# Kernel optimization log

Measured on AMD Instinct MI355X. Metric: run time of the kernel, lower is better.

Reference implementation:

```python
import jax, jax.numpy as jnp
import numpy as np

RADIUS = 0.1
MAX_EDGES = 4_194_304  # cap on total neighbor pairs (expected ~1.1M)

def _cdist(a, b):
    # pairwise Euclidean distances: [M,3] x [N,3] -> [M,N]
    a2 = jnp.sum(a * a, axis=-1, keepdims=True)          # [M,1]
    b2 = jnp.sum(b * b, axis=-1, keepdims=True).T        # [1,N]
    d2 = a2 + b2 - 2.0 * (a @ b.T)
    return jnp.sqrt(jnp.maximum(d2, 0.0))


def setup_inputs() -> dict:
    key = jax.random.key(0)
    k1, k2 = jax.random.split(key)
    inp_positions = jax.random.uniform(k1, (16384, 3), dtype=jnp.float32)
    out_positions = jax.random.uniform(k2, (16384, 3), dtype=jnp.float32)
    return {"inp_positions": inp_positions, "out_positions": out_positions}


def reference(inp_positions, out_positions):
    M = out_positions.shape[0]
    N = inp_positions.shape[0]
    distances = _cdist(out_positions, inp_positions)      # [M,N]
    mask = distances <= RADIUS                            # [M,N] bool
    # jit-compatible nonzero: flatten, fixed-size output, sentinel fill M*N
    flat_idx = jnp.nonzero(mask.ravel(), size=MAX_EDGES, fill_value=M * N)[0]
    query_index = flat_idx // N                           # padded slots -> M (out of range sentinel)
    neighbors_index = jnp.where(flat_idx < M * N, flat_idx % N, -1)
    # bincount(query_index, minlength=M) == row-wise sum of mask
    counts = jnp.sum(mask, axis=1)                        # [M] int32
    row_splits = jnp.pad(jnp.cumsum(counts), (1, 0))      # [M+1]
    return neighbors_index, row_splits
```

## Files before the change

kernel.cpp:

```cpp
#include <hip/hip_runtime.h>
#include <math.h>

typedef float f32x2 __attribute__((ext_vector_type(2)));

constexpr int M_ROWS    = 16384;
constexpr int N_PTS     = 16384;
constexpr int MAX_EDGES = 4194304;

constexpr int TPB    = 256;
constexpr int RPT    = 8;
constexpr int NPAIR  = RPT / 2;
constexpr int NCHUNK = 256;
constexpr int CHUNK  = N_PTS / NCHUNK;
constexpr int WPC    = CHUNK / 32;
constexpr int ROWS_PER_BLOCK = TPB * RPT;
constexpr int RB     = M_ROWS / ROWS_PER_BLOCK;
constexpr int CGRP   = 16;
constexpr int NGRP   = NCHUNK / CGRP;

static __device__ __forceinline__ f32x2 pk_fma(f32x2 a, f32x2 b, f32x2 c) {
#if __has_builtin(__builtin_elementwise_fma)
    return __builtin_elementwise_fma(a, b, c);
#else
    f32x2 r; r.x = __fmaf_rn(a.x, b.x, c.x); r.y = __fmaf_rn(a.y, b.y, c.y); return r;
#endif
}

static __device__ __forceinline__ void bitstep(unsigned& m, float t, float tr) {
    asm("v_cmp_le_f32 vcc, %1, %2\n\t"
        "v_addc_co_u32 %0, vcc, %0, %0, vcc"
        : "+v"(m) : "v"(t), "v"(tr) : "vcc");
}

__global__ void __launch_bounds__(TPB)
mask_count_kernel(const float* __restrict__ inp, const float* __restrict__ outp,
                  unsigned* __restrict__ mask, unsigned char* __restrict__ cchunk,
                  float T) {
    int rb = blockIdx.x / NCHUNK;
    int c  = blockIdx.x % NCHUNK;
    int t  = threadIdx.x;
    __shared__ f32x2 sb[CHUNK * 4];
    if (t < CHUNK) {
        int j = c * CHUNK + t;
        float x = inp[j * 3 + 0], y = inp[j * 3 + 1], z = inp[j * 3 + 2];
        float s = __fadd_rn(__fadd_rn(__fmul_rn(x, x), __fmul_rn(y, y)), __fmul_rn(z, z));
        float nx = -2.0f * x, ny = -2.0f * y, nz = -2.0f * z;
        sb[t * 4 + 0] = (f32x2){nx, nx};
        sb[t * 4 + 1] = (f32x2){ny, ny};
        sb[t * 4 + 2] = (f32x2){nz, nz};
        sb[t * 4 + 3] = (f32x2){s, s};
    }
    __syncthreads();
    int row0 = rb * ROWS_PER_BLOCK + t;
    f32x2 ax[NPAIR], ay[NPAIR], az[NPAIR], Tr[NPAIR];
#pragma unroll
    for (int k = 0; k < NPAIR; ++k) {
        int r0 = row0 + (2 * k) * TPB;
        int r1 = row0 + (2 * k + 1) * TPB;
        float x0 = outp[r0 * 3 + 0], y0 = outp[r0 * 3 + 1], z0 = outp[r0 * 3 + 2];
        float x1 = outp[r1 * 3 + 0], y1 = outp[r1 * 3 + 1], z1 = outp[r1 * 3 + 2];
        float w0 = __fadd_rn(__fadd_rn(__fmul_rn(x0, x0), __fmul_rn(y0, y0)), __fmul_rn(z0, z0));
        float w1 = __fadd_rn(__fadd_rn(__fmul_rn(x1, x1), __fmul_rn(y1, y1)), __fmul_rn(z1, z1));
        ax[k] = (f32x2){x0, x1};
        ay[k] = (f32x2){y0, y1};
        az[k] = (f32x2){z0, z1};
        Tr[k] = (f32x2){__fsub_rn(T, w0), __fsub_rn(T, w1)};
    }
    int cnt[RPT];
#pragma unroll
    for (int r = 0; r < RPT; ++r) cnt[r] = 0;
#pragma unroll
    for (int w = 0; w < WPC; ++w) {
        unsigned m[RPT];
#pragma unroll
        for (int r = 0; r < RPT; ++r) m[r] = 0u;
#pragma unroll
        for (int b = 31; b >= 0; --b) {
            int jj = w * 32 + b;
            f32x2 qx = sb[jj * 4 + 0], qy = sb[jj * 4 + 1];
            f32x2 qz = sb[jj * 4 + 2], qw = sb[jj * 4 + 3];
#pragma unroll
            for (int k = 0; k < NPAIR; ++k) {
                f32x2 acc = pk_fma(az[k], qz, qw);
                acc = pk_fma(ay[k], qy, acc);
                acc = pk_fma(ax[k], qx, acc);
                bitstep(m[2 * k + 0], acc.x, Tr[k].x);
                bitstep(m[2 * k + 1], acc.y, Tr[k].y);
            }
        }
#pragma unroll
        for (int r = 0; r < RPT; ++r) {
            mask[(size_t)(c * WPC + w) * M_ROWS + row0 + r * TPB] = m[r];
            cnt[r] += __popc(m[r]);
        }
    }
#pragma unroll
    for (int r = 0; r < RPT; ++r)
        cchunk[(size_t)c * M_ROWS + row0 + r * TPB] = (unsigned char)cnt[r];
}

__global__ void __launch_bounds__(256)
scan_rows_kernel(const unsigned* __restrict__ cc32, unsigned short* __restrict__ cpfxc,
                 int* __restrict__ totals) {
    __shared__ unsigned tile[64][64];
    int row0 = blockIdx.x * 256;
    int t = threadIdx.x;
    int sum = 0;
    for (int c0 = 0; c0 < NCHUNK; c0 += 64) {
        __syncthreads();
        for (int i = t; i < 64 * 64; i += 256) {
            int cl = i >> 6, rw = i & 63;
            tile[cl][rw] = cc32[(size_t)(c0 + cl) * (M_ROWS / 4) + (row0 / 4) + rw];
        }
        __syncthreads();
#pragma unroll 16
        for (int cl = 0; cl < 64; ++cl) {
            int c = c0 + cl;
            if ((c & (CGRP - 1)) == 0)
                cpfxc[(size_t)(c / CGRP) * M_ROWS + row0 + t] = (unsigned short)sum;
            unsigned wv = tile[cl][t >> 2];
            sum += (wv >> ((t & 3) * 8)) & 0xffu;
        }
    }
    totals[row0 + t] = sum;
}

__global__ void __launch_bounds__(1024)
scan_global_kernel(const int* __restrict__ totals, int* __restrict__ row_splits) {
    __shared__ int sp[1024];
    int t = threadIdx.x;
    const int4* t4 = (const int4*)totals;
    int4 v0 = t4[t * 4 + 0], v1 = t4[t * 4 + 1], v2 = t4[t * 4 + 2], v3 = t4[t * 4 + 3];
    int vals[16] = {v0.x, v0.y, v0.z, v0.w, v1.x, v1.y, v1.z, v1.w,
                    v2.x, v2.y, v2.z, v2.w, v3.x, v3.y, v3.z, v3.w};
    int pre[16];
    int s = 0;
#pragma unroll
    for (int k = 0; k < 16; ++k) { pre[k] = s; s += vals[k]; }
    sp[t] = s;
    __syncthreads();
    for (int off = 1; off < 1024; off <<= 1) {
        int v = (t >= off) ? sp[t - off] : 0;
        __syncthreads();
        sp[t] += v;
        __syncthreads();
    }
    int excl = (t == 0) ? 0 : sp[t - 1];
#pragma unroll
    for (int k = 0; k < 16; ++k) row_splits[t * 16 + k] = excl + pre[k];
    if (t == 1023) row_splits[16384] = sp[1023];
}

__global__ void fill_kernel(int4* __restrict__ out4) {
    int i = blockIdx.x * blockDim.x + threadIdx.x;
    out4[i] = make_int4(-1, -1, -1, -1);
}

__global__ void __launch_bounds__(TPB)
emit_mask_kernel(const unsigned* __restrict__ mask, const unsigned short* __restrict__ cpfxc,
                 const int* __restrict__ rs, int* __restrict__ out_idx) {
    int rb  = blockIdx.x / NGRP;
    int cg  = blockIdx.x % NGRP;
    int row = rb * TPB + threadIdx.x;
    int cur = rs[row] + (int)cpfxc[(size_t)cg * M_ROWS + row];
#pragma unroll 4
    for (int c = cg * CGRP; c < (cg + 1) * CGRP; ++c) {
#pragma unroll
        for (int w = 0; w < WPC; ++w) {
            unsigned m = mask[(size_t)(c * WPC + w) * M_ROWS + row];
            int jb = c * CHUNK + w * 32;
            while (m) {
                int b = __ffs(m) - 1;
                out_idx[cur++] = jb + b;
                m &= m - 1;
            }
        }
    }
}

extern "C" void kernel_launch(void* const* d_in, const int* in_sizes, int n_in,
                              void* d_out, int out_size, void* d_ws, size_t ws_size,
                              hipStream_t stream) {
    const float* inp  = (const float*)d_in[0];
    const float* outp = (const float*)d_in[1];
    int* out_idx    = (int*)d_out;
    int* row_splits = out_idx + MAX_EDGES;

    char* ws = (char*)d_ws;
    size_t off = 0;
    unsigned* mask = (unsigned*)(ws + off);
    off += (size_t)M_ROWS * (N_PTS / 32) * 4;
    unsigned char* cchunk = (unsigned char*)(ws + off);
    off += (size_t)M_ROWS * NCHUNK;
    unsigned short* cpfxc = (unsigned short*)(ws + off);
    off += (size_t)M_ROWS * NGRP * 2;
    int* totals = (int*)(ws + off);
    off += (size_t)M_ROWS * 4;
    if (off > ws_size) return;

    double md  = (double)0.1f + ldexp(1.0, -28);
    double m2 = md * md;
    float  T  = (float)m2;
    if ((double)T >= m2) T = nextafterf(T, 0.0f);

    mask_count_kernel<<<dim3(RB * NCHUNK), dim3(TPB), 0, stream>>>(inp, outp, mask, cchunk, T);
    scan_rows_kernel<<<dim3(M_ROWS / 256), dim3(256), 0, stream>>>((const unsigned*)cchunk, cpfxc, totals);
    scan_global_kernel<<<dim3(1), dim3(1024), 0, stream>>>(totals, row_splits);
    fill_kernel<<<dim3(MAX_EDGES / 4 / TPB), dim3(TPB), 0, stream>>>((int4*)out_idx);
    emit_mask_kernel<<<dim3((M_ROWS / TPB) * NGRP), dim3(TPB), 0, stream>>>(mask, cpfxc, row_splits, out_idx);
}
```

Before: 79.42 us.

## Fuse global scan into row scan, merge fill into emit, use packed-FMA asm

The global row-split scan moves into the last finishing block of the row-scan kernel, which detects itself through an atomic counter reset in the mask kernel. The -1 fill of the output is folded into the emit kernel and now writes only the tail slots past the total edge count, instead of a separate kernel writing the whole 16 MB buffer. Two launches are removed. The shared-memory point layout shrinks to one float4 per point, and the distance computation uses inline v_pk_fma_f32 with op_sel to broadcast scalars, replacing the earlier vcc-based bitstep asm with plain compares. This cuts launch overhead and redundant writes, at the cost of relying on a threadfence and last-block pattern.

```diff
diff --git a/kernel.cpp b/kernel.cpp
--- a/kernel.cpp
+++ b/kernel.cpp
@@ -17,38 +17,22 @@
 constexpr int RB     = M_ROWS / ROWS_PER_BLOCK;
 constexpr int CGRP   = 16;
 constexpr int NGRP   = NCHUNK / CGRP;
-
-static __device__ __forceinline__ f32x2 pk_fma(f32x2 a, f32x2 b, f32x2 c) {
-#if __has_builtin(__builtin_elementwise_fma)
-    return __builtin_elementwise_fma(a, b, c);
-#else
-    f32x2 r; r.x = __fmaf_rn(a.x, b.x, c.x); r.y = __fmaf_rn(a.y, b.y, c.y); return r;
-#endif
-}
-
-static __device__ __forceinline__ void bitstep(unsigned& m, float t, float tr) {
-    asm("v_cmp_le_f32 vcc, %1, %2\n\t"
-        "v_addc_co_u32 %0, vcc, %0, %0, vcc"
-        : "+v"(m) : "v"(t), "v"(tr) : "vcc");
-}
+constexpr int NSCANB = M_ROWS / 256;
 
 __global__ void __launch_bounds__(TPB)
 mask_count_kernel(const float* __restrict__ inp, const float* __restrict__ outp,
                   unsigned* __restrict__ mask, unsigned char* __restrict__ cchunk,
-                  float T) {
+                  float T, int* __restrict__ counter) {
+    if (blockIdx.x == 0 && threadIdx.x == 0) *counter = 0;
     int rb = blockIdx.x / NCHUNK;
     int c  = blockIdx.x % NCHUNK;
     int t  = threadIdx.x;
-    __shared__ f32x2 sb[CHUNK * 4];
+    __shared__ float4 sb[CHUNK];
     if (t < CHUNK) {
         int j = c * CHUNK + t;
         float x = inp[j * 3 + 0], y = inp[j * 3 + 1], z = inp[j * 3 + 2];
         float s = __fadd_rn(__fadd_rn(__fmul_rn(x, x), __fmul_rn(y, y)), __fmul_rn(z, z));
-        float nx = -2.0f * x, ny = -2.0f * y, nz = -2.0f * z;
-        sb[t * 4 + 0] = (f32x2){nx, nx};
-        sb[t * 4 + 1] = (f32x2){ny, ny};
-        sb[t * 4 + 2] = (f32x2){nz, nz};
-        sb[t * 4 + 3] = (f32x2){s, s};
+        sb[t] = make_float4(-2.0f * x, -2.0f * y, -2.0f * z, s);
     }
     __syncthreads();
     int row0 = rb * ROWS_PER_BLOCK + t;
@@ -76,16 +60,19 @@
         for (int r = 0; r < RPT; ++r) m[r] = 0u;
 #pragma unroll
         for (int b = 31; b >= 0; --b) {
-            int jj = w * 32 + b;
-            f32x2 qx = sb[jj * 4 + 0], qy = sb[jj * 4 + 1];
-            f32x2 qz = sb[jj * 4 + 2], qw = sb[jj * 4 + 3];
+            union { float4 f4; f32x2 h[2]; } qu;
+            qu.f4 = sb[w * 32 + b];
+            f32x2 qxy = qu.h[0], qzw = qu.h[1];
 #pragma unroll
             for (int k = 0; k < NPAIR; ++k) {
-                f32x2 acc = pk_fma(az[k], qz, qw);
-                acc = pk_fma(ay[k], qy, acc);
-                acc = pk_fma(ax[k], qx, acc);
-                bitstep(m[2 * k + 0], acc.x, Tr[k].x);
-                bitstep(m[2 * k + 1], acc.y, Tr[k].y);
+                f32x2 acc;
+                asm("v_pk_fma_f32 %0, %1, %2, %2 op_sel:[0,0,1] op_sel_hi:[1,0,1]\n\t"
+                    "v_pk_fma_f32 %0, %3, %4, %0 op_sel:[0,1,0]\n\t"
+                    "v_pk_fma_f32 %0, %5, %4, %0 op_sel_hi:[1,0,1]"
+                    : "=&v"(acc)
+                    : "v"(az[k]), "v"(qzw), "v"(ay[k]), "v"(qxy), "v"(ax[k]));
+                m[2 * k + 0] = m[2 * k + 0] * 2u + (unsigned)(acc.x <= Tr[k].x);
+                m[2 * k + 1] = m[2 * k + 1] * 2u + (unsigned)(acc.y <= Tr[k].y);
             }
         }
 #pragma unroll
@@ -101,8 +88,10 @@
 
 __global__ void __launch_bounds__(256)
 scan_rows_kernel(const unsigned* __restrict__ cc32, unsigned short* __restrict__ cpfxc,
-                 int* __restrict__ totals) {
+                 int* __restrict__ totals, int* __restrict__ row_splits,
+                 int* __restrict__ counter) {
     __shared__ unsigned tile[64][64];
+    __shared__ int lastflag;
     int row0 = blockIdx.x * 256;
     int t = threadIdx.x;
     int sum = 0;
@@ -123,41 +112,42 @@
         }
     }
     totals[row0 + t] = sum;
-}
-
-__global__ void __launch_bounds__(1024)
-scan_global_kernel(const int* __restrict__ totals, int* __restrict__ row_splits) {
-    __shared__ int sp[1024];
-    int t = threadIdx.x;
+    __threadfence();
+    if (t == 0) lastflag = (atomicAdd(counter, 1) == NSCANB - 1);
+    __syncthreads();
+    if (!lastflag) return;
+    __threadfence();
+
     const int4* t4 = (const int4*)totals;
-    int4 v0 = t4[t * 4 + 0], v1 = t4[t * 4 + 1], v2 = t4[t * 4 + 2], v3 = t4[t * 4 + 3];
-    int vals[16] = {v0.x, v0.y, v0.z, v0.w, v1.x, v1.y, v1.z, v1.w,
-                    v2.x, v2.y, v2.z, v2.w, v3.x, v3.y, v3.z, v3.w};
-    int pre[16];
     int s = 0;
 #pragma unroll
-    for (int k = 0; k < 16; ++k) { pre[k] = s; s += vals[k]; }
+    for (int i = 0; i < 16; ++i) {
+        int4 v = t4[t * 16 + i];
+        s += v.x + v.y + v.z + v.w;
+    }
+    int* sp = (int*)&tile[0][0];
     sp[t] = s;
     __syncthreads();
-    for (int off = 1; off < 1024; off <<= 1) {
+    for (int off = 1; off < 256; off <<= 1) {
         int v = (t >= off) ? sp[t - off] : 0;
         __syncthreads();
         sp[t] += v;
         __syncthreads();
     }
-    int excl = (t == 0) ? 0 : sp[t - 1];
-#pragma unroll
-    for (int k = 0; k < 16; ++k) row_splits[t * 16 + k] = excl + pre[k];
-    if (t == 1023) row_splits[16384] = sp[1023];
-}
-
-__global__ void fill_kernel(int4* __restrict__ out4) {
-    int i = blockIdx.x * blockDim.x + threadIdx.x;
-    out4[i] = make_int4(-1, -1, -1, -1);
+    int cur = (t == 0) ? 0 : sp[t - 1];
+#pragma unroll
+    for (int i = 0; i < 16; ++i) {
+        int4 v = t4[t * 16 + i];
+        row_splits[t * 64 + i * 4 + 0] = cur; cur += v.x;
+        row_splits[t * 64 + i * 4 + 1] = cur; cur += v.y;
+        row_splits[t * 64 + i * 4 + 2] = cur; cur += v.z;
+        row_splits[t * 64 + i * 4 + 3] = cur; cur += v.w;
+    }
+    if (t == 255) row_splits[16384] = sp[255];
 }
 
 __global__ void __launch_bounds__(TPB)
-emit_mask_kernel(const unsigned* __restrict__ mask, const unsigned short* __restrict__ cpfxc,
+emit_fill_kernel(const unsigned* __restrict__ mask, const unsigned short* __restrict__ cpfxc,
                  const int* __restrict__ rs, int* __restrict__ out_idx) {
     int rb  = blockIdx.x / NGRP;
     int cg  = blockIdx.x % NGRP;
@@ -175,6 +165,15 @@
                 m &= m - 1;
             }
         }
+    }
+    int E = rs[M_ROWS];
+    int total = MAX_EDGES - E;
+    if (total > 0) {
+        int nb  = (M_ROWS / TPB) * NGRP;
+        int per = (total + nb - 1) / nb;
+        int s0  = E + blockIdx.x * per;
+        int e0  = s0 + per; if (e0 > MAX_EDGES) e0 = MAX_EDGES;
+        for (int i = s0 + threadIdx.x; i < e0; i += TPB) out_idx[i] = -1;
     }
 }
 
@@ -196,16 +195,16 @@
     off += (size_t)M_ROWS * NGRP * 2;
     int* totals = (int*)(ws + off);
     off += (size_t)M_ROWS * 4;
+    int* counter = (int*)(ws + off);
+    off += 256;
     if (off > ws_size) return;
 
-    double md  = (double)0.1f + ldexp(1.0, -28);
+    double md = (double)0.1f + ldexp(1.0, -28);
     double m2 = md * md;
     float  T  = (float)m2;
     if ((double)T >= m2) T = nextafterf(T, 0.0f);
 
-    mask_count_kernel<<<dim3(RB * NCHUNK), dim3(TPB), 0, stream>>>(inp, outp, mask, cchunk, T);
-    scan_rows_kernel<<<dim3(M_ROWS / 256), dim3(256), 0, stream>>>((const unsigned*)cchunk, cpfxc, totals);
-    scan_global_kernel<<<dim3(1), dim3(1024), 0, stream>>>(totals, row_splits);
-    fill_kernel<<<dim3(MAX_EDGES / 4 / TPB), dim3(TPB), 0, stream>>>((int4*)out_idx);
-    emit_mask_kernel<<<dim3((M_ROWS / TPB) * NGRP), dim3(TPB), 0, stream>>>(mask, cpfxc, row_splits, out_idx);
-}
+    mask_count_kernel<<<dim3(RB * NCHUNK), dim3(TPB), 0, stream>>>(inp, outp, mask, cchunk, T, counter);
+    scan_rows_kernel<<<dim3(NSCANB), dim3(256), 0, stream>>>((const unsigned*)cchunk, cpfxc, totals, row_splits, counter);
+    emit_fill_kernel<<<dim3((M_ROWS / TPB) * NGRP), dim3(TPB), 0, stream>>>(mask, cpfxc, row_splits, out_idx);
+}
```

After: 137.0 us. 1.73x slower.
